# Performance work log

Measured on AMD Instinct MI355X. Metric: run time of the kernel, lower is better.

## Reference

```python
import jax, jax.numpy as jnp
import numpy as np

H = 2048          # hidden_size
NH = 16           # num_attention_heads
HD = H // NH      # head_dim = 128
RD = HD // 2      # rotary dim = 64
LAT = H // 8      # latent_dim = 256
B, S = 2, 2048
BASE = 10000.0


def rotary_emb(seq_len, dtype=jnp.float32):
    # DeepseekRotaryEmbedding(dim=RD): inv_freq over arange(0, RD, 2)
    inv_freq = 1.0 / (BASE ** (np.arange(0, RD, 2, dtype=np.float32) / RD))  # [RD//2]
    pos = jnp.arange(seq_len, dtype=dtype)
    sincos = pos[:, None] * jnp.asarray(inv_freq, dtype)                     # [S, RD//2]
    return jnp.concatenate([jnp.sin(sincos), jnp.cos(sincos)], axis=-1)      # [S, RD]


def apply_rope(x, emb):
    # x: [B, S, NH, RD]; emb: [S, RD] with sin first half, cos second half
    half = RD // 2
    x1, x2 = x[..., :half], x[..., half:]
    sin = emb[:, None, :half]   # [S, 1, half] broadcast over heads
    cos = emb[:, None, half:]
    return jnp.concatenate([x1 * cos - x2 * sin, x1 * sin + x2 * cos], axis=-1)


def setup_inputs() -> dict:
    key = jax.random.key(0)
    ks = jax.random.split(key, 9)
    def w(k, shape):
        return jax.random.normal(k, shape, dtype=jnp.float32) * (1.0 / np.sqrt(shape[-1]))
    return {
        "hidden_states": jax.random.normal(ks[0], (B, S, H), dtype=jnp.float32),
        "W_kv_d": w(ks[1], (LAT, H)),
        "W_q_d": w(ks[2], (LAT, H)),
        "W_k_u": w(ks[3], (H // 2, LAT)),
        "W_q_u": w(ks[4], (H // 2, LAT)),
        "W_v_u": w(ks[5], (H, LAT)),
        "W_rope_k": w(ks[6], (H // 2, H)),
        "W_rope_q": w(ks[7], (H // 2, LAT)),
        "W_o": w(ks[8], (H, H)),
    }


def reference(hidden_states, W_kv_d, W_q_d, W_k_u, W_q_u, W_v_u, W_rope_k, W_rope_q, W_o):
    x = hidden_states                                   # [B, S, H]
    kv_d = x @ W_kv_d.T                                 # [B, S, LAT]
    q_d = x @ W_q_d.T                                   # [B, S, LAT]
    k_c = (kv_d @ W_k_u.T).reshape(B, S, NH, RD)        # content half of k
    q_c = (q_d @ W_q_u.T).reshape(B, S, NH, RD)
    v = (kv_d @ W_v_u.T).reshape(B, S, NH, HD)
    k_r = (x @ W_rope_k.T).reshape(B, S, NH, RD)
    q_r = (q_d @ W_rope_q.T).reshape(B, S, NH, RD)

    emb = rotary_emb(S, x.dtype)                        # [S, RD]
    q_r = apply_rope(q_r, emb)
    k_r = apply_rope(k_r, emb)

    q = jnp.concatenate([q_c, q_r], axis=-1)            # [B, S, NH, HD]
    k = jnp.concatenate([k_c, k_r], axis=-1)

    scale = 1.0 / np.sqrt(HD)                           # SDPA default scale
    scores = jnp.einsum("bqhd,bkhd->bhqk", q, k) * scale
    causal = jnp.tril(jnp.ones((S, S), dtype=bool))
    scores = jnp.where(causal, scores, jnp.finfo(scores.dtype).min)
    probs = jax.nn.softmax(scores, axis=-1)
    y = jnp.einsum("bhqk,bkhd->bqhd", probs, v).reshape(B, S, H)
    return y @ W_o.T
```

## Files before the change

kernel.cpp:

```cpp
#include <hip/hip_runtime.h>

typedef unsigned short u16;
typedef unsigned int u32;
typedef __attribute__((ext_vector_type(8))) short bf16x8;
typedef __attribute__((ext_vector_type(4))) float f32x4;

#define DEVI static __device__ __forceinline__

DEVI u16 f2b(float f){
  u32 x = __float_as_uint(f);
  return (u16)((x + 0x7fffu + ((x >> 16) & 1u)) >> 16);
}
DEVI float b2f(u16 u){ return __uint_as_float(((u32)u) << 16); }
DEVI float2 up2(u32 u){
  return make_float2(__uint_as_float(u << 16), __uint_as_float(u & 0xffff0000u));
}
DEVI void gload16(const u16* g, u16* l){
  __builtin_amdgcn_global_load_lds((const __attribute__((address_space(1))) void*)g,
                                   (__attribute__((address_space(3))) void*)l,
                                   16, 0, 0);
}

#define QSCALE 0.12751744900929456f

struct CSrc { const float* s[9]; };
__global__ void cvt_all(CSrc cs, u16* __restrict__ xb, u16* __restrict__ wcat){
  int i = blockIdx.x * 256 + threadIdx.x;
  if (i >= 4259840) return;
  const float4* s; int lo, di; uint2* d;
  if (i < 2097152){
    s = (const float4*)cs.s[0]; lo = 0; di = i; d = (uint2*)xb;
  } else {
    int j = i - 2097152; di = j; d = (uint2*)wcat;
    if      (j <  131072){ s = (const float4*)cs.s[1]; lo = 0;       }
    else if (j <  262144){ s = (const float4*)cs.s[2]; lo = 131072;  }
    else if (j <  786432){ s = (const float4*)cs.s[3]; lo = 262144;  }
    else if (j <  851968){ s = (const float4*)cs.s[4]; lo = 786432;  }
    else if (j <  917504){ s = (const float4*)cs.s[5]; lo = 851968;  }
    else if (j <  983040){ s = (const float4*)cs.s[6]; lo = 917504;  }
    else if (j < 1114112){ s = (const float4*)cs.s[7]; lo = 983040;  }
    else                 { s = (const float4*)cs.s[8]; lo = 1114112; }
  }
  float4 f = s[di - lo];
  u32 a = (u32)f2b(f.x) | ((u32)f2b(f.y) << 16);
  u32 b = (u32)f2b(f.z) | ((u32)f2b(f.w) << 16);
  d[di] = make_uint2(a, b);
}

template<int MODE>
__global__ __launch_bounds__(256, 2)
void gemm_bt(const u16* __restrict__ A, int lda, const u16* __restrict__ W,
             void* __restrict__ D, int N, int K){
  __shared__ u16 As[128 * 32];
  __shared__ u16 Bs[128 * 32];
  const int tid = threadIdx.x;
  const int wave = tid >> 6, lane = tid & 63;
  const int lr = lane & 15, lk = lane >> 4;
  int bid = blockIdx.y * gridDim.x + blockIdx.x;
  const int nwg = gridDim.x * gridDim.y;
  bid = (bid & 7) * (nwg >> 3) + (bid >> 3);
  const int bx = bid % gridDim.x, by = bid / gridDim.x;
  const int m0 = by * 128, n0 = bx * 128;
  const int wm = wave >> 1, wn = wave & 1;
  f32x4 acc[4][4] = {};

  const u16* a0 = A + (size_t)(m0 + (tid >> 2)) * lda + (tid & 3) * 8;
  const u16* a1 = a0 + (size_t)64 * lda;
  const u16* b0 = W + (size_t)(n0 + (tid >> 2)) * K + (tid & 3) * 8;
  const u16* b1 = b0 + (size_t)64 * K;
  u16* lA0 = As + wave * 512;  u16* lA1 = As + 2048 + wave * 512;
  u16* lB0 = Bs + wave * 512;  u16* lB1 = Bs + 2048 + wave * 512;

  for (int k0 = 0; k0 < K; k0 += 32){
    __syncthreads();
    gload16(a0 + k0, lA0);
    gload16(a1 + k0, lA1);
    gload16(b0 + k0, lB0);
    gload16(b1 + k0, lB1);
    asm volatile("s_waitcnt vmcnt(0)" ::: "memory");
    __syncthreads();
    bf16x8 af[4], bfr[4];
    #pragma unroll
    for (int i = 0; i < 4; i++)
      af[i] = *(const bf16x8*)(As + (wm * 64 + i * 16 + lr) * 32 + lk * 8);
    #pragma unroll
    for (int j = 0; j < 4; j++)
      bfr[j] = *(const bf16x8*)(Bs + (wn * 64 + j * 16 + lr) * 32 + lk * 8);
    #pragma unroll
    for (int i = 0; i < 4; i++)
      #pragma unroll
      for (int j = 0; j < 4; j++)
        acc[i][j] = __builtin_amdgcn_mfma_f32_16x16x32_bf16(af[i], bfr[j], acc[i][j], 0, 0, 0);
  }

  const int rb = (lane >> 4) * 4, cl = lane & 15;
  #pragma unroll
  for (int i = 0; i < 4; i++){
    #pragma unroll
    for (int j = 0; j < 4; j++){
      const int mb = m0 + wm * 64 + i * 16 + rb;
      const int n  = n0 + wn * 64 + j * 16 + cl;
      #pragma unroll
      for (int r = 0; r < 4; r++){
        int m = mb + r;
        float v = acc[i][j][r];
        if (MODE == 0) ((u16*)D)[(size_t)m * N + n] = f2b(v);
        else           ((float*)D)[(size_t)m * N + n] = v;
      }
    }
  }
}

__global__ __launch_bounds__(256, 2)
void gemm_up(const u16* __restrict__ dcat, const u16* __restrict__ qW,
             const u16* __restrict__ kvW, u16* __restrict__ qbuf,
             u16* __restrict__ qrp, u16* __restrict__ kbuf, u16* __restrict__ vt){
  __shared__ u16 As[128 * 32];
  __shared__ u16 Bs[128 * 32];
  const int tid = threadIdx.x;
  const int wave = tid >> 6, lane = tid & 63;
  const int lr = lane & 15, lk = lane >> 4;
  int bid = blockIdx.y * 40 + blockIdx.x;
  bid = (bid & 7) * 160 + (bid >> 3);
  const int bx = bid % 40, by = bid / 40;
  const bool qside = bx < 16;
  const u16* A = qside ? dcat + 256 : dcat;
  const u16* W = qside ? qW : kvW;
  const int n0 = (qside ? bx : bx - 16) * 128;
  const int m0 = by * 128;
  const int wm = wave >> 1, wn = wave & 1;
  f32x4 acc[4][4] = {};

  const u16* a0 = A + (size_t)(m0 + (tid >> 2)) * 1536 + (tid & 3) * 8;
  const u16* a1 = a0 + (size_t)64 * 1536;
  const u16* b0 = W + (size_t)(n0 + (tid >> 2)) * 256 + (tid & 3) * 8;
  const u16* b1 = b0 + (size_t)64 * 256;
  u16* lA0 = As + wave * 512;  u16* lA1 = As + 2048 + wave * 512;
  u16* lB0 = Bs + wave * 512;  u16* lB1 = Bs + 2048 + wave * 512;

  for (int k0 = 0; k0 < 256; k0 += 32){
    __syncthreads();
    gload16(a0 + k0, lA0);
    gload16(a1 + k0, lA1);
    gload16(b0 + k0, lB0);
    gload16(b1 + k0, lB1);
    asm volatile("s_waitcnt vmcnt(0)" ::: "memory");
    __syncthreads();
    bf16x8 af[4], bfr[4];
    #pragma unroll
    for (int i = 0; i < 4; i++)
      af[i] = *(const bf16x8*)(As + (wm * 64 + i * 16 + lr) * 32 + lk * 8);
    #pragma unroll
    for (int j = 0; j < 4; j++)
      bfr[j] = *(const bf16x8*)(Bs + (wn * 64 + j * 16 + lr) * 32 + lk * 8);
    #pragma unroll
    for (int i = 0; i < 4; i++)
      #pragma unroll
      for (int j = 0; j < 4; j++)
        acc[i][j] = __builtin_amdgcn_mfma_f32_16x16x32_bf16(af[i], bfr[j], acc[i][j], 0, 0, 0);
  }

  const int rb = (lane >> 4) * 4, cl = lane & 15;
  #pragma unroll
  for (int i = 0; i < 4; i++){
    #pragma unroll
    for (int j = 0; j < 4; j++){
      const int mb = m0 + wm * 64 + i * 16 + rb;
      const int n  = n0 + wn * 64 + j * 16 + cl;
      if (!qside && n >= 1024){
        int n1 = n - 1024, h = n1 >> 7, d = n1 & 127, b = mb >> 11, s = mb & 2047;
        u32 lo = (u32)f2b(acc[i][j][0]) | ((u32)f2b(acc[i][j][1]) << 16);
        u32 hi = (u32)f2b(acc[i][j][2]) | ((u32)f2b(acc[i][j][3]) << 16);
        *(uint2*)(vt + (((size_t)(b * 16 + h) * 128 + d) * 2048 + s)) = make_uint2(lo, hi);
      } else {
        #pragma unroll
        for (int r = 0; r < 4; r++){
          int m = mb + r;
          float v = acc[i][j][r];
          if (qside){
            if (n < 1024){
              qrp[(size_t)m * 1024 + n] = f2b(v);
            } else {
              int n1 = n - 1024, h = n1 >> 6, d = n1 & 63;
              qbuf[(((size_t)(m >> 11) * 16 + h) * 2048 + (m & 2047)) * 128 + d] = f2b(v * QSCALE);
            }
          } else {
            int h = n >> 6, d = n & 63;
            kbuf[(((size_t)(m >> 11) * 16 + h) * 2048 + (m & 2047)) * 128 + d] = f2b(v);
          }
        }
      }
    }
  }
}

__global__ void rope_k(const u16* __restrict__ qrp, const u16* __restrict__ dcat,
                       u16* __restrict__ Qb, u16* __restrict__ Kb){
  int idx = blockIdx.x * 256 + threadIdx.x;
  if (idx >= (1 << 21)) return;
  int j = idx & 31, h = (idx >> 5) & 15, s = (idx >> 9) & 2047, b = (idx >> 20) & 1;
  float inv = exp2f((float)j * (-13.287712379549449f / 32.0f));
  float ang = (float)s * inv;
  float sn = sinf(ang), cs = cosf(ang);
  size_t soq = ((size_t)(b * 2048 + s)) * 1024 + h * 64 + j;
  size_t sok = ((size_t)(b * 2048 + s)) * 1536 + 512 + h * 64 + j;
  size_t dd = (((size_t)(b * 16 + h)) * 2048 + s) * 128;
  {
    float x1 = b2f(qrp[soq]), x2 = b2f(qrp[soq + 32]);
    Qb[dd + 64 + j] = f2b((x1 * cs - x2 * sn) * QSCALE);
    Qb[dd + 96 + j] = f2b((x1 * sn + x2 * cs) * QSCALE);
  }
  {
    float x1 = b2f(dcat[sok]), x2 = b2f(dcat[sok + 32]);
    Kb[dd + 64 + j] = f2b(x1 * cs - x2 * sn);
    Kb[dd + 96 + j] = f2b(x1 * sn + x2 * cs);
  }
}

__global__ __launch_bounds__(512, 1)
void flash_part(const u16* __restrict__ Q, const u16* __restrict__ K,
                const u16* __restrict__ VT, u16* __restrict__ Op0,
                u16* __restrict__ Op1, float2* __restrict__ ML){
  __shared__ u16 k_s[3][8192];
  __shared__ u16 v_s[8192];
  __shared__ u16 p_s[8][2048];
  const int tid = threadIdx.x;
  const int w = tid >> 6, l = tid & 63;
  const int lr = l & 15, hk = l >> 4;
  const int bh = blockIdx.x;
  const int qt = 7 - blockIdx.y;
  const int z  = blockIdx.z;
  const int b = bh >> 4, h = bh & 15;
  const size_t base = (size_t)bh * 2048 * 128;
  const u16* Qb = Q + base;
  const u16* Kb = K + base;
  const u16* Vb = VT + base;
  u16* myp = p_s[w];
  const int q0 = qt * 256 + w * 32;
  const int T  = 2 * qt + 2;
  const int t0 = z * T;

  bf16x8 qa[2][4];
  #pragma unroll
  for (int mi = 0; mi < 2; mi++)
    #pragma unroll
    for (int ks = 0; ks < 4; ks++)
      qa[mi][ks] = *(const bf16x8*)(Qb + (size_t)(q0 + mi * 16 + lr) * 128 + ks * 32 + hk * 8);

  f32x4 o[2][8] = {};
  float mbase[2] = {-1e30f, -1e30f};
  float lsum[2] = {0.f, 0.f};

  auto STAGE_K = [&](int kt, int buf){
    #pragma unroll
    for (int it = 0; it < 2; ++it){
      int row = it * 32 + w * 4 + (l >> 4);
      gload16(Kb + (size_t)(kt * 64 + row) * 128 + (((l & 15) ^ (row & 15)) << 3),
              &k_s[buf][it * 4096 + w * 512]);
    }
  };
  auto STAGE_V = [&](int kt){
    #pragma unroll
    for (int it = 0; it < 2; ++it){
      int d = it * 64 + w * 8 + (l >> 3);
      gload16(Vb + (size_t)d * 2048 + kt * 64 + (((l & 7) ^ (d & 7)) << 3),
              &v_s[it * 4096 + w * 512]);
    }
  };

  STAGE_K(t0, 0);
  STAGE_K(t0 + 1, 1);
  asm volatile("s_waitcnt vmcnt(2)" ::: "memory");
  __builtin_amdgcn_s_barrier();

  for (int tt = 0; tt < T; ++tt){
    const int t = t0 + tt;
    STAGE_V(t);
    const bool pre2 = (tt + 2 < T);
    if (pre2) STAGE_K(t + 2, (tt + 2) % 3);

    const bool act = (t * 64 <= q0 + 31);
    if (act){
      const u16* ks_ = k_s[tt % 3];
      f32x4 sc[2][4] = {};
      #pragma unroll
      for (int ksd = 0; ksd < 4; ++ksd){
        bf16x8 kb[4];
        #pragma unroll
        for (int nj = 0; nj < 4; ++nj){
          int row = nj * 16 + lr;
          kb[nj] = *(const bf16x8*)(ks_ + row * 128 + (((ksd * 4 + hk) ^ lr) << 3));
        }
        __builtin_amdgcn_s_setprio(1);
        #pragma unroll
        for (int mi = 0; mi < 2; ++mi)
          #pragma unroll
          for (int nj = 0; nj < 4; ++nj)
            sc[mi][nj] = __builtin_amdgcn_mfma_f32_16x16x32_bf16(kb[nj], qa[mi][ksd], sc[mi][nj], 0, 0, 0);
        __builtin_amdgcn_s_setprio(0);
      }
      float lmax[2] = {-3e38f, -3e38f};
      if (t * 64 + 63 > q0){
        #pragma unroll
        for (int mi = 0; mi < 2; ++mi){
          int qrow = q0 + mi * 16 + lr;
          #pragma unroll
          for (int nj = 0; nj < 4; ++nj)
            #pragma unroll
            for (int r = 0; r < 4; ++r){
              int kc = t * 64 + nj * 16 + hk * 4 + r;
              float s = (kc <= qrow) ? sc[mi][nj][r] : -1e30f;
              sc[mi][nj][r] = s;
              lmax[mi] = fmaxf(lmax[mi], s);
            }
        }
      } else {
        #pragma unroll
        for (int mi = 0; mi < 2; ++mi)
          #pragma unroll
          for (int nj = 0; nj < 4; ++nj)
            #pragma unroll
            for (int r = 0; r < 4; ++r)
              lmax[mi] = fmaxf(lmax[mi], sc[mi][nj][r]);
      }
      if (__any((lmax[0] > mbase[0] + 8.f) || (lmax[1] > mbase[1] + 8.f))){
        #pragma unroll
        for (int mi = 0; mi < 2; ++mi){
          float mx = lmax[mi];
          mx = fmaxf(mx, __shfl_xor(mx, 16));
          mx = fmaxf(mx, __shfl_xor(mx, 32));
          float mnew = fmaxf(mbase[mi], mx);
          float alpha = exp2f(mbase[mi] - mnew);
          mbase[mi] = mnew;
          lsum[mi] *= alpha;
          #pragma unroll
          for (int dj = 0; dj < 8; ++dj)
            #pragma unroll
            for (int r = 0; r < 4; ++r) o[mi][dj][r] *= alpha;
        }
      }
      #pragma unroll
      for (int mi = 0; mi < 2; ++mi){
        u16* prow = myp + (mi * 16 + lr) * 64;
        float rs = 0.f;
        #pragma unroll
        for (int nj = 0; nj < 4; ++nj){
          float p0 = exp2f(sc[mi][nj][0] - mbase[mi]);
          float p1 = exp2f(sc[mi][nj][1] - mbase[mi]);
          float p2 = exp2f(sc[mi][nj][2] - mbase[mi]);
          float p3 = exp2f(sc[mi][nj][3] - mbase[mi]);
          rs += (p0 + p1) + (p2 + p3);
          u32 a = (u32)f2b(p0) | ((u32)f2b(p1) << 16);
          u32 c = (u32)f2b(p2) | ((u32)f2b(p3) << 16);
          *(uint2*)(prow + ((nj * 16 + hk * 4) ^ ((lr & 7) << 3))) = make_uint2(a, c);
        }
        lsum[mi] += rs;
      }
    }

    if (pre2) asm volatile("s_waitcnt vmcnt(2)" ::: "memory");
    else      asm volatile("s_waitcnt vmcnt(0)" ::: "memory");
    __builtin_amdgcn_s_barrier();
    asm volatile("s_waitcnt lgkmcnt(0)" ::: "memory");
    __builtin_amdgcn_sched_barrier(0);

    if (act){
      #pragma unroll
      for (int kk = 0; kk < 2; ++kk){
        bf16x8 pb[2], va[8];
        #pragma unroll
        for (int mi = 0; mi < 2; ++mi)
          pb[mi] = *(const bf16x8*)(myp + (mi * 16 + lr) * 64 +
                     ((kk * 32 + hk * 8) ^ ((lr & 7) << 3)));
        #pragma unroll
        for (int dj = 0; dj < 8; ++dj){
          int d = dj * 16 + lr;
          va[dj] = *(const bf16x8*)(&v_s[d * 64 + (((kk * 4 + hk) ^ (lr & 7)) << 3)]);
        }
        __builtin_amdgcn_s_setprio(1);
        #pragma unroll
        for (int mi = 0; mi < 2; ++mi)
          #pragma unroll
          for (int dj = 0; dj < 8; ++dj)
            o[mi][dj] = __builtin_amdgcn_mfma_f32_16x16x32_bf16(va[dj], pb[mi], o[mi][dj], 0, 0, 0);
        __builtin_amdgcn_s_setprio(0);
      }
    }

    __builtin_amdgcn_s_barrier();
  }

  u16* Op = z ? Op1 : Op0;
  u16* scr = myp;
  #pragma unroll
  for (int mi = 0; mi < 2; ++mi){
    float lt = lsum[mi];
    lt += __shfl_xor(lt, 16);
    lt += __shfl_xor(lt, 32);
    if (hk == 0){
      float2 v; v.x = mbase[mi]; v.y = lt;
      ML[((size_t)z * 32 + bh) * 2048 + qt * 256 + w * 32 + mi * 16 + lr] = v;
    }
    #pragma unroll
    for (int dj = 0; dj < 8; ++dj){
      u32 a = (u32)f2b(o[mi][dj][0]) | ((u32)f2b(o[mi][dj][1]) << 16);
      u32 c = (u32)f2b(o[mi][dj][2]) | ((u32)f2b(o[mi][dj][3]) << 16);
      *(uint2*)(scr + lr * 128 + ((dj * 16 + hk * 4) ^ ((lr & 7) << 3))) = make_uint2(a, c);
    }
    asm volatile("s_waitcnt lgkmcnt(0)" ::: "memory");
    __builtin_amdgcn_sched_barrier(0);
    #pragma unroll
    for (int rr = 0; rr < 4; ++rr){
      int row = rr * 4 + hk;
      uint4 vv = *(const uint4*)(scr + row * 128 + ((lr * 8) ^ ((row & 7) << 3)));
      *(uint4*)(Op + ((size_t)(b * 2048) + qt * 256 + w * 32 + mi * 16 + row) * 2048
                    + h * 128 + lr * 8) = vv;
    }
    asm volatile("s_waitcnt lgkmcnt(0)" ::: "memory");
    __builtin_amdgcn_sched_barrier(0);
  }
}

__global__ void merge_k(const u16* __restrict__ Op0, const u16* __restrict__ Op1,
                        const float2* __restrict__ ML, u16* __restrict__ Y){
  int i = blockIdx.x * 256 + threadIdx.x;
  if (i >= (1 << 20)) return;
  int row = i >> 8;
  int c8 = (i & 255) << 3;
  int b = row >> 11, s = row & 2047, h = c8 >> 7;
  int bh = b * 16 + h;
  float2 ml0 = ML[(size_t)bh * 2048 + s];
  float2 ml1 = ML[(size_t)(32 + bh) * 2048 + s];
  float m = fmaxf(ml0.x, ml1.x);
  float w0 = exp2f(ml0.x - m), w1 = exp2f(ml1.x - m);
  float inv = 1.0f / fmaxf(ml0.y * w0 + ml1.y * w1, 1e-30f);
  size_t off = (size_t)row * 2048 + c8;
  uint4 a = *(const uint4*)(Op0 + off);
  uint4 c = *(const uint4*)(Op1 + off);
  u32 res[4];
  u32 au[4] = {a.x, a.y, a.z, a.w};
  u32 cu[4] = {c.x, c.y, c.z, c.w};
  #pragma unroll
  for (int j = 0; j < 4; ++j){
    float2 f = up2(au[j]), g = up2(cu[j]);
    float r0 = (f.x * w0 + g.x * w1) * inv;
    float r1 = (f.y * w0 + g.y * w1) * inv;
    res[j] = (u32)f2b(r0) | ((u32)f2b(r1) << 16);
  }
  *(uint4*)(Y + off) = make_uint4(res[0], res[1], res[2], res[3]);
}

extern "C" void kernel_launch(void* const* d_in, const int* in_sizes, int n_in,
                              void* d_out, int out_size, void* d_ws, size_t ws_size,
                              hipStream_t stream){
  u16* p = (u16*)d_ws;
  auto alloc = [&](size_t n){ u16* r = p; p += n; return r; };
  u16* wcat = alloc(8650752);
  u16* downW  = wcat;
  u16* qcatW  = wcat + 3145728;
  u16* kvcatW = wcat + 3670016;
  u16* wo     = wcat + 4456448;
  u16* xb   = alloc(8388608);
  u16* dcat = alloc(6291456);
  u16* qrp  = alloc(4194304);
  u16* qbuf = alloc(8388608);
  u16* kbuf = alloc(8388608);
  u16* vt   = alloc(8388608);
  u16* ybuf = alloc(8388608);
  float2* ml = (float2*)alloc(524288);

  CSrc cs;
  cs.s[0] = (const float*)d_in[0];
  cs.s[1] = (const float*)d_in[1];
  cs.s[2] = (const float*)d_in[2];
  cs.s[3] = (const float*)d_in[6];
  cs.s[4] = (const float*)d_in[7];
  cs.s[5] = (const float*)d_in[4];
  cs.s[6] = (const float*)d_in[3];
  cs.s[7] = (const float*)d_in[5];
  cs.s[8] = (const float*)d_in[8];
  cvt_all<<<16640, 256, 0, stream>>>(cs, xb, wcat);

  dim3 blk(256);
  gemm_bt<0><<<dim3(12, 32), blk, 0, stream>>>(xb, 2048, downW, dcat, 1536, 2048);
  gemm_up<<<dim3(40, 32), blk, 0, stream>>>(dcat, qcatW, kvcatW, qbuf, qrp, kbuf, vt);
  rope_k<<<(1 << 21) / 256, 256, 0, stream>>>(qrp, dcat, qbuf, kbuf);
  u16* op0 = xb;
  u16* op1 = dcat;
  flash_part<<<dim3(32, 8, 2), dim3(512), 0, stream>>>(qbuf, kbuf, vt, op0, op1, ml);
  merge_k<<<4096, 256, 0, stream>>>(op0, op1, ml, ybuf);
  gemm_bt<3><<<dim3(16, 32), blk, 0, stream>>>(ybuf, 2048, wo, d_out, 2048, 2048);
}
```

Before: 214.0 us.

## Prefetch V one tile ahead with triple buffering and drop trailing barrier

V tiles are moved into a three-deep LDS ring and loaded one iteration ahead, so V loads overlap the QK^T and softmax work instead of being issued and waited on in the same iteration. The wait counts are adjusted for the extra in-flight loads, and the end-of-iteration barrier is removed because ring buffers are no longer overwritten while still being read. The bf16 packing of probabilities switches to a cheaper round-half-up pack. The cost is more LDS use and slightly different rounding of P.

```diff
diff --git a/kernel.cpp b/kernel.cpp
--- a/kernel.cpp
+++ b/kernel.cpp
@@ -14,6 +14,11 @@
 DEVI float b2f(u16 u){ return __uint_as_float(((u32)u) << 16); }
 DEVI float2 up2(u32 u){
   return make_float2(__uint_as_float(u << 16), __uint_as_float(u & 0xffff0000u));
+}
+DEVI u32 pk2(float a, float b){
+  u32 ua = __float_as_uint(a) + 0x8000u;
+  u32 ub = __float_as_uint(b) + 0x8000u;
+  return (ua >> 16) | (ub & 0xffff0000u);
 }
 DEVI void gload16(const u16* g, u16* l){
   __builtin_amdgcn_global_load_lds((const __attribute__((address_space(1))) void*)g,
@@ -222,7 +227,7 @@
                 const u16* __restrict__ VT, u16* __restrict__ Op0,
                 u16* __restrict__ Op1, float2* __restrict__ ML){
   __shared__ u16 k_s[3][8192];
-  __shared__ u16 v_s[8192];
+  __shared__ u16 v_s[3][8192];
   __shared__ u16 p_s[8][2048];
   const int tid = threadIdx.x;
   const int w = tid >> 6, l = tid & 63;
@@ -259,15 +264,16 @@
               &k_s[buf][it * 4096 + w * 512]);
     }
   };
-  auto STAGE_V = [&](int kt){
+  auto STAGE_V = [&](int kt, int buf){
     #pragma unroll
     for (int it = 0; it < 2; ++it){
       int d = it * 64 + w * 8 + (l >> 3);
       gload16(Vb + (size_t)d * 2048 + kt * 64 + (((l & 7) ^ (d & 7)) << 3),
-              &v_s[it * 4096 + w * 512]);
+              &v_s[buf][it * 4096 + w * 512]);
     }
   };
 
+  STAGE_V(t0, 0);
   STAGE_K(t0, 0);
   STAGE_K(t0 + 1, 1);
   asm volatile("s_waitcnt vmcnt(2)" ::: "memory");
@@ -275,9 +281,10 @@
 
   for (int tt = 0; tt < T; ++tt){
     const int t = t0 + tt;
-    STAGE_V(t);
-    const bool pre2 = (tt + 2 < T);
-    if (pre2) STAGE_K(t + 2, (tt + 2) % 3);
+    const bool preV = (tt + 1 < T);
+    const bool preK = (tt + 2 < T);
+    if (preV) STAGE_V(t + 1, (tt + 1) % 3);
+    if (preK) STAGE_K(t + 2, (tt + 2) % 3);
 
     const bool act = (t * 64 <= q0 + 31);
     if (act){
@@ -350,21 +357,22 @@
           float p2 = exp2f(sc[mi][nj][2] - mbase[mi]);
           float p3 = exp2f(sc[mi][nj][3] - mbase[mi]);
           rs += (p0 + p1) + (p2 + p3);
-          u32 a = (u32)f2b(p0) | ((u32)f2b(p1) << 16);
-          u32 c = (u32)f2b(p2) | ((u32)f2b(p3) << 16);
-          *(uint2*)(prow + ((nj * 16 + hk * 4) ^ ((lr & 7) << 3))) = make_uint2(a, c);
+          *(uint2*)(prow + ((nj * 16 + hk * 4) ^ ((lr & 7) << 3))) =
+              make_uint2(pk2(p0, p1), pk2(p2, p3));
         }
         lsum[mi] += rs;
       }
     }
 
-    if (pre2) asm volatile("s_waitcnt vmcnt(2)" ::: "memory");
-    else      asm volatile("s_waitcnt vmcnt(0)" ::: "memory");
+    if (preK)      asm volatile("s_waitcnt vmcnt(4)" ::: "memory");
+    else if (preV) asm volatile("s_waitcnt vmcnt(2)" ::: "memory");
+    else           asm volatile("s_waitcnt vmcnt(0)" ::: "memory");
     __builtin_amdgcn_s_barrier();
     asm volatile("s_waitcnt lgkmcnt(0)" ::: "memory");
     __builtin_amdgcn_sched_barrier(0);
 
     if (act){
+      const u16* vs_ = v_s[tt % 3];
       #pragma unroll
       for (int kk = 0; kk < 2; ++kk){
         bf16x8 pb[2], va[8];
@@ -375,7 +383,7 @@
         #pragma unroll
         for (int dj = 0; dj < 8; ++dj){
           int d = dj * 16 + lr;
-          va[dj] = *(const bf16x8*)(&v_s[d * 64 + (((kk * 4 + hk) ^ (lr & 7)) << 3)]);
+          va[dj] = *(const bf16x8*)(vs_ + d * 64 + (((kk * 4 + hk) ^ (lr & 7)) << 3));
         }
         __builtin_amdgcn_s_setprio(1);
         #pragma unroll
@@ -386,8 +394,6 @@
         __builtin_amdgcn_s_setprio(0);
       }
     }
-
-    __builtin_amdgcn_s_barrier();
   }
 
   u16* Op = z ? Op1 : Op0;
```

Result: no change. 211.6 us (-1.1%).
